# Kernel optimization log

Measured on AMD Instinct MI355X. Metric: run time of the kernel, lower is better.

The kernel has to match this reference:

```python
import jax, jax.numpy as jnp
import numpy as np

B, D, H, V = 64, 1024, 8, 32000
OFF = 0  # pad/ignore token id
W_BCE, W_LB, W_ENT, W_BUDGET = 1.0, 0.2, 0.01, 0.05


def setup_inputs() -> dict:
    key = jax.random.key(0)
    ks = jax.random.split(key, 6)
    hidden = jax.random.normal(ks[0], (B, D), dtype=jnp.float32)
    router_w1 = jax.random.normal(ks[1], (4 * D, D), dtype=jnp.float32) * 0.02
    router_b1 = jnp.zeros((4 * D,), dtype=jnp.float32)
    router_w2 = jax.random.normal(ks[2], (H, 4 * D), dtype=jnp.float32) * 0.02
    router_b2 = jnp.zeros((H,), dtype=jnp.float32)
    heads_w = jax.random.normal(ks[3], (H, D, V), dtype=jnp.float32) * 0.02
    labels = jax.random.randint(ks[4], (B, H), 0, V, dtype=jnp.int64)
    return {
        'hidden': hidden,
        'router_w1': router_w1, 'router_b1': router_b1,
        'router_w2': router_w2, 'router_b2': router_b2,
        'heads_w': heads_w,
        'labels': labels,
        'k_max': 2,
    }


def reference(hidden, router_w1, router_b1, router_w2, router_b2, heads_w, labels, k_max):
    nH = router_b2.shape[0]
    # Router: Linear -> exact GELU -> Linear
    r = jax.nn.gelu(hidden @ router_w1.T + router_b1, approximate=False)
    gate_logits = r @ router_w2.T + router_b2              # [B, H]
    # Eval routing: top-k -> active mask (one_hot(topk).sum(2).bool())
    _, topk = jax.lax.top_k(gate_logits, k_max)            # [B, k]
    active = jnp.sum(jax.nn.one_hot(topk, nH, dtype=jnp.int32), axis=1) > 0  # [B, H]
    # All H heads applied to the same hidden state -> single fused GEMM
    logits = jnp.einsum('bd,hdv->bhv', hidden, heads_w)    # [B, H, V]
    # Masked cross-entropy with ignore_index == OFF (mean over valid entries)
    logp = jax.nn.log_softmax(logits, axis=-1)
    nll = -jnp.take_along_axis(logp, labels[:, :, None], axis=-1)[..., 0]  # [B, H]
    valid = active & (labels != OFF)
    n_valid = jnp.maximum(jnp.sum(valid), 1)
    ce = jnp.sum(jnp.where(valid, nll, 0.0)) / n_valid
    # BCE-with-logits against active mask (teacher_mask=None path)
    tgt = active.astype(jnp.float32)
    g = gate_logits
    bce = jnp.mean(jnp.maximum(g, 0.0) - g * tgt + jnp.log1p(jnp.exp(-jnp.abs(g))))
    # Load-balance
    freq = tgt.mean(axis=0)
    lb = jnp.sum((freq - 1.0 / nH) ** 2)
    # Router entropy
    p = jax.nn.softmax(g, axis=-1)
    ent = -jnp.mean(jnp.sum(p * jnp.log(p + 1e-9), axis=-1))
    budget = tgt.mean()
    loss = ce + W_BCE * bce + W_LB * lb + W_ENT * ent + W_BUDGET * budget
    return logits, gate_logits, active, loss
```

## Files before the change

### kernel.cpp

```cpp
#include <hip/hip_runtime.h>
#include <cstdint>
#include <cstddef>

#define BB 64
#define DD 1024
#define HH 8
#define VV 32000
#define H4 4096
#define BM 256
#define BK 32
#define NBLK 125

#define OFF_HHI    0
#define OFF_HLO    32768
#define OFF_R      65536
#define OFF_NLL    327680
#define OFF_CNT    328192
#define OFF_SCAL   328704
#define OFF_PMAX   330000
#define OFF_PSUM   394000

#define OFF_LOGITS 0
#define OFF_GATE   16384000
#define OFF_ACT    16384512
#define OFF_LOSS   16385024

typedef __attribute__((ext_vector_type(8))) _Float16 f16x8;
typedef __attribute__((ext_vector_type(4))) float f32x4;

__global__ void k_h2f16split(const float* __restrict__ in,
                             _Float16* __restrict__ hi_out,
                             _Float16* __restrict__ lo_out) {
    int i = blockIdx.x * 256 + threadIdx.x;
    float x = in[i];
    _Float16 hi = (_Float16)x;
    hi_out[i] = hi;
    lo_out[i] = (_Float16)(x - (float)hi);
}

__global__ __launch_bounds__(64) void k_router1(
    const float* __restrict__ w1, const _Float16* __restrict__ hhi,
    const _Float16* __restrict__ hlo, const float* __restrict__ b1,
    float* __restrict__ r) {
    const int j0 = blockIdx.x * 16;
    const int lane = threadIdx.x;
    const int lg = lane >> 4, lr = lane & 15;
    const float* wp = w1 + (size_t)(j0 + lr) * DD + lg * 8;

    f32x4 acc[4];
#pragma unroll
    for (int nt = 0; nt < 4; ++nt) acc[nt] = (f32x4){0.f, 0.f, 0.f, 0.f};

    for (int kc = 0; kc < DD; kc += 32) {
        float4 a0 = *(const float4*)(wp + kc);
        float4 a1 = *(const float4*)(wp + kc + 4);
        float av[8] = {a0.x, a0.y, a0.z, a0.w, a1.x, a1.y, a1.z, a1.w};
        f16x8 fahi, falo;
#pragma unroll
        for (int j = 0; j < 8; ++j) {
            _Float16 h16 = (_Float16)av[j];
            fahi[j] = h16;
            falo[j] = (_Float16)(av[j] - (float)h16);
        }
#pragma unroll
        for (int nt = 0; nt < 4; ++nt) {
            size_t boff = (size_t)(nt * 16 + lr) * DD + kc + lg * 8;
            f16x8 fbhi = *(const f16x8*)(hhi + boff);
            f16x8 fblo = *(const f16x8*)(hlo + boff);
            acc[nt] = __builtin_amdgcn_mfma_f32_16x16x32_f16(fahi, fbhi, acc[nt], 0, 0, 0);
            acc[nt] = __builtin_amdgcn_mfma_f32_16x16x32_f16(fahi, fblo, acc[nt], 0, 0, 0);
            acc[nt] = __builtin_amdgcn_mfma_f32_16x16x32_f16(falo, fbhi, acc[nt], 0, 0, 0);
        }
    }

#pragma unroll
    for (int nt = 0; nt < 4; ++nt) {
        int b = nt * 16 + lr;
        int j = j0 + lg * 4;
        float4 o;
        float* ov = (float*)&o;
#pragma unroll
        for (int q = 0; q < 4; ++q) {
            float s = acc[nt][q] + b1[j + q];
            ov[q] = 0.5f * s * (1.0f + erff(s * 0.70710678118654752f));
        }
        *(float4*)&r[(size_t)b * H4 + j] = o;
    }
}

__global__ void k_router2(const float* __restrict__ r, const float* __restrict__ w2,
                          const float* __restrict__ b2, float* __restrict__ gate) {
    int b = blockIdx.x;
    int h = threadIdx.x >> 5;
    int lane = threadIdx.x & 31;
    const float* rr = r + (size_t)b * H4;
    const float* ww = w2 + (size_t)h * H4;
    float s = 0.f;
    for (int j = lane; j < H4; j += 32) s = fmaf(rr[j], ww[j], s);
    for (int off = 16; off > 0; off >>= 1) s += __shfl_down(s, off, 32);
    if (lane == 0) gate[b * HH + h] = s + b2[h];
}

__global__ void k_routing_aux(const float* __restrict__ gate, const int* __restrict__ kmaxp,
                              float* __restrict__ act_out, float* __restrict__ scal) {
    __shared__ float af[64][8];
    __shared__ float bces[64], ents[64];
    int b = threadIdx.x;
    float g[8];
#pragma unroll
    for (int h = 0; h < 8; ++h) g[h] = gate[b * 8 + h];
    int k = kmaxp[0]; k = k < 0 ? 0 : (k > 8 ? 8 : k);
    bool act[8] = {false, false, false, false, false, false, false, false};
    for (int s = 0; s < k; ++s) {
        int best = -1; float bv = -1e30f;
#pragma unroll
        for (int h = 0; h < 8; ++h)
            if (!act[h] && g[h] > bv) { bv = g[h]; best = h; }
        act[best] = true;
    }
    float m = -1e30f;
#pragma unroll
    for (int h = 0; h < 8; ++h) m = fmaxf(m, g[h]);
    float se = 0.f, ex[8];
#pragma unroll
    for (int h = 0; h < 8; ++h) { ex[h] = expf(g[h] - m); se += ex[h]; }
    float bce = 0.f, ent = 0.f;
#pragma unroll
    for (int h = 0; h < 8; ++h) {
        float t = act[h] ? 1.f : 0.f;
        bce += fmaxf(g[h], 0.f) - g[h] * t + log1pf(expf(-fabsf(g[h])));
        float p = ex[h] / se;
        ent -= p * logf(p + 1e-9f);
        af[b][h] = t;
        act_out[b * 8 + h] = t;
    }
    bces[b] = bce; ents[b] = ent;
    __syncthreads();
    if (b == 0) {
        float bsum = 0.f, esum = 0.f, asum = 0.f, lb = 0.f;
        for (int i = 0; i < 64; ++i) { bsum += bces[i]; esum += ents[i]; }
        for (int h = 0; h < 8; ++h) {
            float f = 0.f;
            for (int i = 0; i < 64; ++i) f += af[i][h];
            asum += f;
            float fr = f / 64.f - 0.125f;
            lb += fr * fr;
        }
        scal[0] = bsum / 512.f;
        scal[1] = lb;
        scal[2] = esum / 64.f;
        scal[3] = asum / 512.f;
    }
}

__global__ __launch_bounds__(256, 4) void k_heads_gemm(
    const float* __restrict__ W, const _Float16* __restrict__ hA,
    float* __restrict__ out, float* __restrict__ pmax, float* __restrict__ psum) {
    __shared__ __align__(16) float ldsA[BK][256];
    const int bid = blockIdx.x;
    const int h   = bid & 7;
    const int blk = bid >> 3;
    const int v0  = blk * BM;
    const int tid = threadIdx.x;
    const int wv = tid >> 6, lane = tid & 63;
    const int lg = lane >> 4, lr = lane & 15;

    const float* wbase = W + (size_t)h * DD * VV + v0;

    f32x4 acc[4][4];
#pragma unroll
    for (int vt = 0; vt < 4; ++vt)
#pragma unroll
        for (int nt = 0; nt < 4; ++nt) acc[vt][nt] = (f32x4){0.f, 0.f, 0.f, 0.f};

    for (int kc = 0; kc < DD / BK; ++kc) {
#pragma unroll
        for (int i_ = 0; i_ < 8; ++i_) {
            int r_ = wv + 4 * i_;
            const float* src_ = wbase + (size_t)(kc * BK + r_) * VV
                                + ((lane ^ (r_ >> 3)) << 2);
            __builtin_amdgcn_global_load_lds(
                (const __attribute__((address_space(1))) unsigned int*)src_,
                (__attribute__((address_space(3))) unsigned int*)&ldsA[r_][0],
                16, 0, 2 );
        }
        asm volatile("s_waitcnt vmcnt(0)" ::: "memory");
        asm volatile("s_barrier" ::: "memory");

        f16x8 fb[4];
#pragma unroll
        for (int nt = 0; nt < 4; ++nt)
            fb[nt] = *(const f16x8*)(hA + (size_t)(nt * 16 + lr) * DD + kc * BK + lg * 8);

        const int vq_base = wv * 16 + (lr >> 2);
#pragma unroll
        for (int vt = 0; vt < 4; ++vt) {
            const int p = (vq_base + vt * 4) ^ lg;
            const float* col = &ldsA[lg * 8][(p << 2) + (lr & 3)];
            f16x8 fa;
#pragma unroll
            for (int j = 0; j < 8; ++j) fa[j] = (_Float16)col[j * 256];
#pragma unroll
            for (int nt = 0; nt < 4; ++nt)
                acc[vt][nt] = __builtin_amdgcn_mfma_f32_16x16x32_f16(fa, fb[nt], acc[vt][nt], 0, 0, 0);
        }

        asm volatile("s_waitcnt lgkmcnt(0)" ::: "memory");
        asm volatile("s_barrier" ::: "memory");
    }

    float* sm = &ldsA[0][0];
#pragma unroll
    for (int pass = 0; pass < 2; ++pass) {
#pragma unroll
        for (int nt2 = 0; nt2 < 2; ++nt2) {
            int nt = pass * 2 + nt2;
            int b = nt * 16 + lr;
            int brow = nt2 * 16 + lr;
#pragma unroll
            for (int vt = 0; vt < 4; ++vt) {
                int vcol = wv * 64 + vt * 16 + lg * 4;
                int col = vcol ^ ((b & 7) << 2);
                *(f32x4*)&sm[brow * 256 + col] = acc[vt][nt];
            }
        }
        __syncthreads();
#pragma unroll
        for (int i = 0; i < 8; ++i) {
            int fid = tid + i * 256;
            int brow = fid >> 6;
            int c4 = fid & 63;
            int b = pass * 32 + brow;
            int col = (c4 * 4) ^ ((b & 7) << 2);
            f32x4 vv = *(const f32x4*)&sm[brow * 256 + col];
            __builtin_nontemporal_store(vv, (f32x4*)&out[((size_t)b * HH + h) * VV + v0 + c4 * 4]);
            float mx = fmaxf(fmaxf(vv[0], vv[1]), fmaxf(vv[2], vv[3]));
#pragma unroll
            for (int off = 32; off > 0; off >>= 1)
                mx = fmaxf(mx, __shfl_xor(mx, off));
            float se = expf(vv[0] - mx) + expf(vv[1] - mx) + expf(vv[2] - mx) + expf(vv[3] - mx);
#pragma unroll
            for (int off = 32; off > 0; off >>= 1)
                se += __shfl_xor(se, off);
            if (lane == 0) {
                pmax[(size_t)(b * HH + h) * NBLK + blk] = mx;
                psum[(size_t)(b * HH + h) * NBLK + blk] = se;
            }
        }
        __syncthreads();
    }
}

__global__ __launch_bounds__(64) void k_ce_finish(
    const float* __restrict__ pmax, const float* __restrict__ psum,
    const float* __restrict__ logits, const float* __restrict__ act,
    const int* __restrict__ labels, float* __restrict__ nllv, float* __restrict__ cnt) {
    int p = blockIdx.x;
    int lane = threadIdx.x;
    float m = -1e30f, s = 0.f;
    for (int i = lane; i < NBLK; i += 64) {
        float m2 = pmax[(size_t)p * NBLK + i];
        float s2 = psum[(size_t)p * NBLK + i];
        float M = fmaxf(m, m2);
        s = s * expf(m - M) + s2 * expf(m2 - M);
        m = M;
    }
#pragma unroll
    for (int off = 32; off > 0; off >>= 1) {
        float m2 = __shfl_xor(m, off);
        float s2 = __shfl_xor(s, off);
        float M = fmaxf(m, m2);
        s = s * expf(m - M) + s2 * expf(m2 - M);
        m = M;
    }
    if (lane == 0) {
        int lab = labels[p];
        float lv = logits[(size_t)p * VV + lab];
        float nll = -(lv - m - logf(s));
        bool valid = (act[p] > 0.5f) && (lab != 0);
        nllv[p] = valid ? nll : 0.f;
        cnt[p]  = valid ? 1.f : 0.f;
    }
}

__global__ void k_final_loss(const float* __restrict__ nllv, const float* __restrict__ cnt,
                             const float* __restrict__ scal, float* __restrict__ lossp) {
    __shared__ float r1[256], r2[256];
    float a = nllv[threadIdx.x] + nllv[threadIdx.x + 256];
    float c = cnt[threadIdx.x]  + cnt[threadIdx.x + 256];
    r1[threadIdx.x] = a; r2[threadIdx.x] = c; __syncthreads();
    for (int s = 128; s > 0; s >>= 1) {
        if (threadIdx.x < s) { r1[threadIdx.x] += r1[threadIdx.x + s]; r2[threadIdx.x] += r2[threadIdx.x + s]; }
        __syncthreads();
    }
    if (threadIdx.x == 0) {
        float nv = r2[0] < 1.f ? 1.f : r2[0];
        float ce = r1[0] / nv;
        lossp[0] = ce + 1.0f * scal[0] + 0.2f * scal[1] + 0.01f * scal[2] + 0.05f * scal[3];
    }
}

extern "C" void kernel_launch(void* const* d_in, const int* in_sizes, int n_in,
                              void* d_out, int out_size, void* d_ws, size_t ws_size,
                              hipStream_t stream) {
    const float* hidden = (const float*)d_in[0];
    const float* w1     = (const float*)d_in[1];
    const float* b1     = (const float*)d_in[2];
    const float* w2     = (const float*)d_in[3];
    const float* b2     = (const float*)d_in[4];
    const float* W      = (const float*)d_in[5];
    const int*   labels = (const int*)d_in[6];
    const int*   kmaxp  = (const int*)d_in[7];

    float* ws  = (float*)d_ws;
    float* out = (float*)d_out;

    _Float16* hhi = (_Float16*)(ws + OFF_HHI);
    _Float16* hlo = (_Float16*)(ws + OFF_HLO);
    float* r     = ws + OFF_R;
    float* nllv  = ws + OFF_NLL;
    float* cntv  = ws + OFF_CNT;
    float* scal  = ws + OFF_SCAL;
    float* pmax  = ws + OFF_PMAX;
    float* psum  = ws + OFF_PSUM;

    float* logits = out + OFF_LOGITS;
    float* gate   = out + OFF_GATE;
    float* activ  = out + OFF_ACT;
    float* lossp  = out + OFF_LOSS;

    k_h2f16split<<<dim3(256), 256, 0, stream>>>(hidden, hhi, hlo);
    k_router1<<<dim3(256), 64, 0, stream>>>(w1, hhi, hlo, b1, r);
    k_router2<<<dim3(64), 256, 0, stream>>>(r, w2, b2, gate);
    k_routing_aux<<<dim3(1), 64, 0, stream>>>(gate, kmaxp, activ, scal);
    k_heads_gemm<<<dim3(NBLK * 8), 256, 0, stream>>>(W, hhi, logits, pmax, psum);
    k_ce_finish<<<dim3(512), 64, 0, stream>>>(pmax, psum, logits, activ, labels, nllv, cntv);
    k_final_loss<<<dim3(1), 256, 0, stream>>>(nllv, cntv, scal, lossp);
}
```

Before: 305.2 us.

## Double-buffer heads GEMM with wider 512-column tiles and smaller K step

Reworks the heads GEMM so each block covers 512 vocab columns instead of 256, with a last block that overlaps its neighbour to handle the 32000 remainder. K tiles shrink to 16 and are staged into two LDS buffers, so the next tile's global-to-LDS load runs while the current tile feeds the MFMAs. This removes one of the two barriers per K step. The MFMA shape changes to 16x16x16, the per-block softmax partials are split into two halves, and the duplicated tail half is skipped in the CE reduction. Risks are higher register pressure (twice the accumulators, launch bounds lowered to 2 waves per SIMD), fewer blocks in the grid, and unswizzled LDS reads that may cause bank conflicts.

```diff
diff --git a/kernel.cpp b/kernel.cpp
--- a/kernel.cpp
+++ b/kernel.cpp
@@ -7,9 +7,11 @@
 #define HH 8
 #define VV 32000
 #define H4 4096
-#define BM 256
-#define BK 32
-#define NBLK 125
+#define BM2 512
+#define BK2 16
+#define NB2 63
+#define LST 516
+#define NPART 126
 
 #define OFF_HHI    0
 #define OFF_HLO    32768
@@ -18,7 +20,7 @@
 #define OFF_CNT    328192
 #define OFF_SCAL   328704
 #define OFF_PMAX   330000
-#define OFF_PSUM   394000
+#define OFF_PSUM   394512
 
 #define OFF_LOGITS 0
 #define OFF_GATE   16384000
@@ -26,6 +28,7 @@
 #define OFF_LOSS   16385024
 
 typedef __attribute__((ext_vector_type(8))) _Float16 f16x8;
+typedef __attribute__((ext_vector_type(4))) _Float16 f16x4;
 typedef __attribute__((ext_vector_type(4))) float f32x4;
 
 __global__ void k_h2f16split(const float* __restrict__ in,
@@ -153,60 +156,73 @@
     }
 }
 
-__global__ __launch_bounds__(256, 4) void k_heads_gemm(
+__global__ __launch_bounds__(256, 2) void k_heads_gemm(
     const float* __restrict__ W, const _Float16* __restrict__ hA,
     float* __restrict__ out, float* __restrict__ pmax, float* __restrict__ psum) {
-    __shared__ __align__(16) float ldsA[BK][256];
+    __shared__ __align__(16) float ldsA[2][BK2 * LST];
     const int bid = blockIdx.x;
     const int h   = bid & 7;
     const int blk = bid >> 3;
-    const int v0  = blk * BM;
+    const int v0  = (blk == NB2 - 1) ? (VV - BM2) : blk * BM2;
+    const bool tail = (blk == NB2 - 1);
     const int tid = threadIdx.x;
     const int wv = tid >> 6, lane = tid & 63;
     const int lg = lane >> 4, lr = lane & 15;
 
     const float* wbase = W + (size_t)h * DD * VV + v0;
 
-    f32x4 acc[4][4];
-#pragma unroll
-    for (int vt = 0; vt < 4; ++vt)
+#define STAGE(kc_, buf_)                                                        \
+    {                                                                           \
+        _Pragma("unroll")                                                       \
+        for (int i_ = 0; i_ < 4; ++i_) {                                        \
+            int r_ = wv + 4 * i_;                                               \
+            _Pragma("unroll")                                                   \
+            for (int hh_ = 0; hh_ < 2; ++hh_) {                                 \
+                const float* src_ = wbase + (size_t)((kc_) * BK2 + r_) * VV     \
+                                    + hh_ * 256 + lane * 4;                     \
+                __builtin_amdgcn_global_load_lds(                               \
+                    (const __attribute__((address_space(1))) unsigned int*)src_,\
+                    (__attribute__((address_space(3))) unsigned int*)           \
+                        &ldsA[buf_][r_ * LST + hh_ * 256],                      \
+                    16, 0, 2 );                                    \
+            }                                                                   \
+        }                                                                       \
+    }
+
+    f32x4 acc[8][4];
+#pragma unroll
+    for (int vt = 0; vt < 8; ++vt)
 #pragma unroll
         for (int nt = 0; nt < 4; ++nt) acc[vt][nt] = (f32x4){0.f, 0.f, 0.f, 0.f};
 
-    for (int kc = 0; kc < DD / BK; ++kc) {
-#pragma unroll
-        for (int i_ = 0; i_ < 8; ++i_) {
-            int r_ = wv + 4 * i_;
-            const float* src_ = wbase + (size_t)(kc * BK + r_) * VV
-                                + ((lane ^ (r_ >> 3)) << 2);
-            __builtin_amdgcn_global_load_lds(
-                (const __attribute__((address_space(1))) unsigned int*)src_,
-                (__attribute__((address_space(3))) unsigned int*)&ldsA[r_][0],
-                16, 0, 2 );
-        }
+    STAGE(0, 0);
+    asm volatile("s_waitcnt vmcnt(0)" ::: "memory");
+    __syncthreads();
+
+    for (int kc = 0; kc < DD / BK2; ++kc) {
+        const int cur = kc & 1;
+
+        f16x4 fb[4];
+#pragma unroll
+        for (int nt = 0; nt < 4; ++nt)
+            fb[nt] = *(const f16x4*)(hA + (size_t)(nt * 16 + lr) * DD + kc * BK2 + lg * 4);
+
+        if (kc < DD / BK2 - 1) STAGE(kc + 1, cur ^ 1);
+
+#pragma unroll
+        for (int vt = 0; vt < 8; ++vt) {
+            const int col = wv * 128 + vt * 16 + lr;
+            f16x4 fa;
+#pragma unroll
+            for (int j = 0; j < 4; ++j)
+                fa[j] = (_Float16)ldsA[cur][(lg * 4 + j) * LST + col];
+#pragma unroll
+            for (int nt = 0; nt < 4; ++nt)
+                acc[vt][nt] = __builtin_amdgcn_mfma_f32_16x16x16f16(fa, fb[nt], acc[vt][nt], 0, 0, 0);
+        }
+
         asm volatile("s_waitcnt vmcnt(0)" ::: "memory");
-        asm volatile("s_barrier" ::: "memory");
-
-        f16x8 fb[4];
-#pragma unroll
-        for (int nt = 0; nt < 4; ++nt)
-            fb[nt] = *(const f16x8*)(hA + (size_t)(nt * 16 + lr) * DD + kc * BK + lg * 8);
-
-        const int vq_base = wv * 16 + (lr >> 2);
-#pragma unroll
-        for (int vt = 0; vt < 4; ++vt) {
-            const int p = (vq_base + vt * 4) ^ lg;
-            const float* col = &ldsA[lg * 8][(p << 2) + (lr & 3)];
-            f16x8 fa;
-#pragma unroll
-            for (int j = 0; j < 8; ++j) fa[j] = (_Float16)col[j * 256];
-#pragma unroll
-            for (int nt = 0; nt < 4; ++nt)
-                acc[vt][nt] = __builtin_amdgcn_mfma_f32_16x16x32_f16(fa, fb[nt], acc[vt][nt], 0, 0, 0);
-        }
-
-        asm volatile("s_waitcnt lgkmcnt(0)" ::: "memory");
-        asm volatile("s_barrier" ::: "memory");
+        __syncthreads();
     }
 
     float* sm = &ldsA[0][0];
@@ -218,37 +234,41 @@
             int b = nt * 16 + lr;
             int brow = nt2 * 16 + lr;
 #pragma unroll
-            for (int vt = 0; vt < 4; ++vt) {
-                int vcol = wv * 64 + vt * 16 + lg * 4;
+            for (int vt = 0; vt < 8; ++vt) {
+                int vcol = wv * 128 + vt * 16 + lg * 4;
                 int col = vcol ^ ((b & 7) << 2);
-                *(f32x4*)&sm[brow * 256 + col] = acc[vt][nt];
+                *(f32x4*)&sm[brow * LST + col] = acc[vt][nt];
             }
         }
         __syncthreads();
 #pragma unroll
-        for (int i = 0; i < 8; ++i) {
+        for (int i = 0; i < 16; ++i) {
             int fid = tid + i * 256;
-            int brow = fid >> 6;
-            int c4 = fid & 63;
+            int brow = fid >> 7;
+            int c4 = fid & 127;
             int b = pass * 32 + brow;
             int col = (c4 * 4) ^ ((b & 7) << 2);
-            f32x4 vv = *(const f32x4*)&sm[brow * 256 + col];
+            f32x4 vv = *(const f32x4*)&sm[brow * LST + col];
             __builtin_nontemporal_store(vv, (f32x4*)&out[((size_t)b * HH + h) * VV + v0 + c4 * 4]);
-            float mx = fmaxf(fmaxf(vv[0], vv[1]), fmaxf(vv[2], vv[3]));
-#pragma unroll
-            for (int off = 32; off > 0; off >>= 1)
-                mx = fmaxf(mx, __shfl_xor(mx, off));
-            float se = expf(vv[0] - mx) + expf(vv[1] - mx) + expf(vv[2] - mx) + expf(vv[3] - mx);
-#pragma unroll
-            for (int off = 32; off > 0; off >>= 1)
-                se += __shfl_xor(se, off);
-            if (lane == 0) {
-                pmax[(size_t)(b * HH + h) * NBLK + blk] = mx;
-                psum[(size_t)(b * HH + h) * NBLK + blk] = se;
+            int half = (wv & 1);
+            if (!(tail && half == 0)) {
+                float mx = fmaxf(fmaxf(vv[0], vv[1]), fmaxf(vv[2], vv[3]));
+#pragma unroll
+                for (int off = 32; off > 0; off >>= 1)
+                    mx = fmaxf(mx, __shfl_xor(mx, off));
+                float se = expf(vv[0] - mx) + expf(vv[1] - mx) + expf(vv[2] - mx) + expf(vv[3] - mx);
+#pragma unroll
+                for (int off = 32; off > 0; off >>= 1)
+                    se += __shfl_xor(se, off);
+                if (lane == 0) {
+                    pmax[(size_t)(b * HH + h) * NPART + blk * 2 + half] = mx;
+                    psum[(size_t)(b * HH + h) * NPART + blk * 2 + half] = se;
+                }
             }
         }
         __syncthreads();
     }
+#undef STAGE
 }
 
 __global__ __launch_bounds__(64) void k_ce_finish(
@@ -258,9 +278,10 @@
     int p = blockIdx.x;
     int lane = threadIdx.x;
     float m = -1e30f, s = 0.f;
-    for (int i = lane; i < NBLK; i += 64) {
-        float m2 = pmax[(size_t)p * NBLK + i];
-        float s2 = psum[(size_t)p * NBLK + i];
+    for (int i = lane; i < NPART; i += 64) {
+        if (i == (NB2 - 1) * 2) continue;
+        float m2 = pmax[(size_t)p * NPART + i];
+        float s2 = psum[(size_t)p * NPART + i];
         float M = fmaxf(m, m2);
         s = s * expf(m - M) + s2 * expf(m2 - M);
         m = M;
@@ -333,7 +354,7 @@
     k_router1<<<dim3(256), 64, 0, stream>>>(w1, hhi, hlo, b1, r);
     k_router2<<<dim3(64), 256, 0, stream>>>(r, w2, b2, gate);
     k_routing_aux<<<dim3(1), 64, 0, stream>>>(gate, kmaxp, activ, scal);
-    k_heads_gemm<<<dim3(NBLK * 8), 256, 0, stream>>>(W, hhi, logits, pmax, psum);
+    k_heads_gemm<<<dim3(NB2 * 8), 256, 0, stream>>>(W, hhi, logits, pmax, psum);
     k_ce_finish<<<dim3(512), 64, 0, stream>>>(pmax, psum, logits, activ, labels, nllv, cntv);
     k_final_loss<<<dim3(1), 256, 0, stream>>>(nllv, cntv, scal, lossp);
 }
```

After: 295.4 us. 1.03x faster.
